# Kernel tuning notes

Hardware: AMD Instinct MI355X
Metric: run time of the kernel (lower is better)

Reference implementation:

```python
import jax, jax.numpy as jnp
import numpy as np

N = 50000        # nodes
E = 1_600_000    # edges
F_IN = 128
HID = 128
OUT = 128
NEG_SLOPE = 0.2  # PyG GATConv default


def _gat_layer(x, src, dst, W, a_src, a_dst, b, n_nodes):
    """PyG GATConv (heads=1, add_self_loops handled by caller)."""
    h = x @ W                                   # [N, d_out]
    alpha_src = h @ a_src                       # [N]
    alpha_dst = h @ a_dst                       # [N]
    e = jax.nn.leaky_relu(alpha_src[src] + alpha_dst[dst], NEG_SLOPE)  # [E']
    # segment softmax over incoming edges of each destination node
    m = jax.ops.segment_max(e, dst, num_segments=n_nodes)
    e = jnp.exp(e - m[dst])
    s = jax.ops.segment_sum(e, dst, num_segments=n_nodes)
    alpha = e / s[dst]                          # [E']
    out = jax.ops.segment_sum(alpha[:, None] * h[src], dst, num_segments=n_nodes)
    return out + b


def setup_inputs() -> dict:
    key = jax.random.key(0)
    ks = jax.random.split(key, 11)
    sW1 = 1.0 / np.sqrt(F_IN)
    sW2 = 1.0 / np.sqrt(HID)
    return {
        "x": jax.random.normal(ks[0], (N, F_IN), dtype=jnp.float32),
        "edge_index": jax.random.randint(ks[1], (2, E), 0, N, dtype=jnp.int64
                                         if jax.config.jax_enable_x64 else jnp.int32),
        "W1": jax.random.normal(ks[2], (F_IN, HID), dtype=jnp.float32) * sW1,
        "a1_src": jax.random.normal(ks[3], (HID,), dtype=jnp.float32) * sW2,
        "a1_dst": jax.random.normal(ks[4], (HID,), dtype=jnp.float32) * sW2,
        "b1": jnp.zeros((HID,), dtype=jnp.float32),
        "W2": jax.random.normal(ks[5], (HID, OUT), dtype=jnp.float32) * sW2,
        "a2_src": jax.random.normal(ks[6], (OUT,), dtype=jnp.float32) * sW2,
        "a2_dst": jax.random.normal(ks[7], (OUT,), dtype=jnp.float32) * sW2,
        "b2": jnp.zeros((OUT,), dtype=jnp.float32),
    }


def reference(x, edge_index, W1, a1_src, a1_dst, b1, W2, a2_src, a2_dst, b2):
    n = x.shape[0]
    loop = jnp.arange(n, dtype=edge_index.dtype)
    src = jnp.concatenate([edge_index[0], loop])   # add self loops (PyG default)
    dst = jnp.concatenate([edge_index[1], loop])
    h = _gat_layer(x, src, dst, W1, a1_src, a1_dst, b1, n)
    h = jax.nn.relu(h)
    # F.dropout with training=False is identity (eval-mode reference)
    out = _gat_layer(h, src, dst, W2, a2_src, a2_dst, b2, n)
    return out
```

## Files before the change

### kernel.cpp

```cpp
#include <hip/hip_runtime.h>
#include <hip/hip_bf16.h>
#include <hip/hip_fp16.h>

#define FD 128
#define CBW 128
#define NBK 512

typedef _Float16 half8 __attribute__((ext_vector_type(8)));
typedef float f32x4 __attribute__((ext_vector_type(4)));

__global__ __launch_bounds__(256) void k_wz(const float* __restrict__ W1,
                                            const float* __restrict__ W2,
                                            __half* __restrict__ T1,
                                            __half* __restrict__ T2,
                                            int* __restrict__ ccnt, int nb) {
    const int t = threadIdx.x;
    if (blockIdx.x == 2) {
        for (int i = t; i < nb; i += 256) ccnt[i] = 0;
        return;
    }
    __shared__ float sw[128 * 129];
    const float* W = blockIdx.x ? W2 : W1;
    __half* T = blockIdx.x ? T2 : T1;
#pragma unroll
    for (int i = 0; i < 64; i++) {
        int idx = i * 256 + t;
        sw[(idx >> 7) * 129 + (idx & 127)] = W[idx];
    }
    __syncthreads();
#pragma unroll
    for (int i = 0; i < 32; i++) {
        int o = i * 256 + t;
        int c = o >> 6, kp = o & 63;
        float lo = sw[(kp * 2) * 129 + c];
        float hi = sw[(kp * 2 + 1) * 129 + c];
        *(__half2*)&T[c * 128 + kp * 2] = __floats2half2_rn(lo, hi);
    }
}

__global__ __launch_bounds__(256) void k_pg(const int* __restrict__ dst,
                                            int* __restrict__ ccnt, int e, int nb,
                                            const float* __restrict__ X,
                                            const __half* __restrict__ Wt,
                                            const float* __restrict__ a_s,
                                            const float* __restrict__ a_d,
                                            __half* __restrict__ H,
                                            float* __restrict__ as_,
                                            float* __restrict__ ad_, int n) {
    __shared__ int lh[NBK];
    const int t = threadIdx.x;
    if (blockIdx.x < 256) {
        for (int i = t; i < NBK; i += 256) lh[i] = 0;
        __syncthreads();
        for (int i = blockIdx.x * 256 + t; i < e; i += 256 * 256)
            atomicAdd(&lh[dst[i] >> 7], 1);
        __syncthreads();
        for (int i = t; i < nb; i += 256) {
            int c = lh[i];
            if (c) atomicAdd(&ccnt[i], c);
        }
    } else {
        const int bid = blockIdx.x - 256;
        const int wave = t >> 6, lane = t & 63;
        const int g = lane >> 4, c16 = lane & 15;
        const int row0 = bid * 64 + wave * 16;

        half8 A[4];
        {
            int row = row0 + c16;
            int rc = (row < n) ? row : (n - 1);
            const float* xp = &X[(size_t)rc * 128 + g * 8];
#pragma unroll
            for (int kc = 0; kc < 4; kc++) {
                float4 x0 = *(const float4*)(xp + kc * 32);
                float4 x1 = *(const float4*)(xp + kc * 32 + 4);
                half8 a;
                a[0] = (_Float16)x0.x; a[1] = (_Float16)x0.y;
                a[2] = (_Float16)x0.z; a[3] = (_Float16)x0.w;
                a[4] = (_Float16)x1.x; a[5] = (_Float16)x1.y;
                a[6] = (_Float16)x1.z; a[7] = (_Float16)x1.w;
                A[kc] = a;
            }
        }
        f32x4 acc[8];
#pragma unroll
        for (int ct = 0; ct < 8; ct++) acc[ct] = (f32x4){0.f, 0.f, 0.f, 0.f};
#pragma unroll
        for (int ct = 0; ct < 8; ct++) {
            const __half* wp = &Wt[(ct * 16 + c16) * 128 + g * 8];
#pragma unroll
            for (int kc = 0; kc < 4; kc++) {
                half8 b = *(const half8*)(wp + kc * 32);
                acc[ct] = __builtin_amdgcn_mfma_f32_16x16x32_f16(A[kc], b, acc[ct], 0, 0, 0);
            }
        }
        float asv[8], adv[8];
#pragma unroll
        for (int ct = 0; ct < 8; ct++) {
            asv[ct] = a_s[ct * 16 + c16];
            adv[ct] = a_d[ct * 16 + c16];
        }
#pragma unroll
        for (int r = 0; r < 4; r++) {
            const int row = row0 + g * 4 + r;
            float vs = 0.f, vd = 0.f;
#pragma unroll
            for (int ct = 0; ct < 8; ct++) {
                float v = acc[ct][r];
                vs += v * asv[ct];
                vd += v * adv[ct];
                if (row < n) H[(size_t)row * 128 + ct * 16 + c16] = __float2half(v);
            }
#pragma unroll
            for (int off = 8; off; off >>= 1) {
                vs += __shfl_xor(vs, off, 16);
                vd += __shfl_xor(vd, off, 16);
            }
            if (c16 == 0 && row < n) { as_[row] = vs; ad_[row] = vd; }
        }
    }
}

__global__ void k_cscan(const int* __restrict__ ccnt, int* __restrict__ cbase,
                        int* __restrict__ ccur, int nb, int* __restrict__ rowptr, int n) {
    __shared__ int wsum[16];
    __shared__ int woff[17];
    const int t = threadIdx.x, lane = t & 63, wid = t >> 6;
    int v = (t < nb) ? ccnt[t] : 0;
    int s = v;
#pragma unroll
    for (int off = 1; off < 64; off <<= 1) {
        int u = __shfl_up(s, off, 64);
        if (lane >= off) s += u;
    }
    if (lane == 63) wsum[wid] = s;
    __syncthreads();
    if (wid == 0) {
        int w2 = (lane < 16) ? wsum[lane] : 0;
#pragma unroll
        for (int off = 1; off < 16; off <<= 1) {
            int u = __shfl_up(w2, off, 64);
            if (lane >= off) w2 += u;
        }
        if (lane < 16) woff[lane + 1] = w2;
        if (lane == 0) woff[0] = 0;
    }
    __syncthreads();
    int excl = woff[wid] + (s - v);
    if (t < nb) { cbase[t] = excl; ccur[t] = excl; }
    if (t == 0) { cbase[nb] = woff[16]; rowptr[n] = woff[16]; }
}

__global__ __launch_bounds__(256) void k_scat(const int* __restrict__ src,
                                              const int* __restrict__ dst,
                                              int* __restrict__ ccur,
                                              int* __restrict__ ebuf,
                                              int e, int nb, int nscat) {
    __shared__ int lh[NBK];
    __shared__ int lb[NBK];
    const int t = threadIdx.x;
    const int per = (e + nscat - 1) / nscat;
    const int lo = blockIdx.x * per;
    const int hi = min(e, lo + per);
    for (int i = t; i < NBK; i += 256) lh[i] = 0;
    __syncthreads();
    for (int i = lo + t; i < hi; i += 256) atomicAdd(&lh[dst[i] >> 7], 1);
    __syncthreads();
    for (int i = t; i < nb; i += 256) {
        int c = lh[i];
        lb[i] = c ? atomicAdd(&ccur[i], c) : 0;
    }
    __syncthreads();
    for (int i = t; i < NBK; i += 256) lh[i] = 0;
    __syncthreads();
    for (int i = lo + t; i < hi; i += 256) {
        int d = dst[i];
        int bkt = d >> 7;
        int r = atomicAdd(&lh[bkt], 1);
        ebuf[lb[bkt] + r] = (src[i] << 7) | (d & (CBW - 1));
    }
}

__global__ __launch_bounds__(256) void k_fine(const int* __restrict__ ebuf,
                                              const int* __restrict__ cbase,
                                              int* __restrict__ rowptr,
                                              int* __restrict__ colidx, int n) {
    const int b = blockIdx.x;
    const int node0 = b * CBW;
    const int nloc = min(CBW, n - node0);
    const int beg = cbase[b], end = cbase[b + 1];
    __shared__ int fh[CBW];
    __shared__ int fo[CBW];
    __shared__ int w0tot;
    const int t = threadIdx.x;
    if (t < CBW) fh[t] = 0;
    __syncthreads();
    for (int e = beg + t; e < end; e += 256) atomicAdd(&fh[ebuf[e] & (CBW - 1)], 1);
    __syncthreads();
    int v = 0, s = 0;
    if (t < CBW) {
        v = fh[t];
        s = v;
#pragma unroll
        for (int off = 1; off < 64; off <<= 1) {
            int u = __shfl_up(s, off, 64);
            if ((t & 63) >= off) s += u;
        }
        if (t == 63) w0tot = s;
    }
    __syncthreads();
    if (t < CBW) fo[t] = ((t >= 64) ? w0tot : 0) + s - v;
    __syncthreads();
    if (t < nloc) rowptr[node0 + t] = beg + fo[t];
    if (t < CBW) fh[t] = 0;
    __syncthreads();
    for (int e = beg + t; e < end; e += 256) {
        int rec = ebuf[e];
        int d = rec & (CBW - 1);
        int r = atomicAdd(&fh[d], 1);
        colidx[beg + fo[d] + r] = rec >> 7;
    }
}

__global__ __launch_bounds__(256) void k_gemm(const __half* __restrict__ X,
                                              const __half* __restrict__ Wt,
                                              const float* __restrict__ a_s,
                                              const float* __restrict__ a_d,
                                              __half* __restrict__ H,
                                              float* __restrict__ as_,
                                              float* __restrict__ ad_, int n) {
    const int t = threadIdx.x;
    const int wave = t >> 6, lane = t & 63;
    const int g = lane >> 4, c16 = lane & 15;
    const int row0 = blockIdx.x * 64 + wave * 16;

    half8 A[4];
    {
        int row = row0 + c16;
        int rc = (row < n) ? row : (n - 1);
        const __half* xp = &X[(size_t)rc * 128 + g * 8];
#pragma unroll
        for (int kc = 0; kc < 4; kc++) A[kc] = *(const half8*)(xp + kc * 32);
    }
    f32x4 acc[8];
#pragma unroll
    for (int ct = 0; ct < 8; ct++) acc[ct] = (f32x4){0.f, 0.f, 0.f, 0.f};
#pragma unroll
    for (int ct = 0; ct < 8; ct++) {
        const __half* wp = &Wt[(ct * 16 + c16) * 128 + g * 8];
#pragma unroll
        for (int kc = 0; kc < 4; kc++) {
            half8 b = *(const half8*)(wp + kc * 32);
            acc[ct] = __builtin_amdgcn_mfma_f32_16x16x32_f16(A[kc], b, acc[ct], 0, 0, 0);
        }
    }
    float asv[8], adv[8];
#pragma unroll
    for (int ct = 0; ct < 8; ct++) {
        asv[ct] = a_s[ct * 16 + c16];
        adv[ct] = a_d[ct * 16 + c16];
    }
#pragma unroll
    for (int r = 0; r < 4; r++) {
        const int row = row0 + g * 4 + r;
        float vs = 0.f, vd = 0.f;
#pragma unroll
        for (int ct = 0; ct < 8; ct++) {
            float v = acc[ct][r];
            vs += v * asv[ct];
            vd += v * adv[ct];
            if (row < n) H[(size_t)row * 128 + ct * 16 + c16] = __float2half(v);
        }
#pragma unroll
        for (int off = 8; off; off >>= 1) {
            vs += __shfl_xor(vs, off, 16);
            vd += __shfl_xor(vd, off, 16);
        }
        if (c16 == 0 && row < n) { as_[row] = vs; ad_[row] = vd; }
    }
}

__device__ __forceinline__ void fmix8(float* acc, uint4 hv, float w) {
    union { uint4 u; _Float16 h[8]; } c;
    c.u = hv;
#pragma unroll
    for (int j = 0; j < 8; j++) acc[j] += w * (float)c.h[j];
}

__global__ __launch_bounds__(256) void k_aggr(const __half* __restrict__ H,
                                              const float* __restrict__ as_,
                                              const float* __restrict__ ad_,
                                              const int* __restrict__ rowptr,
                                              const int* __restrict__ colidx,
                                              const float* __restrict__ bias,
                                              float* __restrict__ outf,
                                              __half* __restrict__ outh,
                                              int n, int mode) {
    __shared__ int2 pr[4][64];
    const int wid = threadIdx.x >> 6;
    const int lane = threadIdx.x & 63;
    const int node = blockIdx.x * 4 + wid;
    if (node >= n) return;
    const int q = lane >> 4;
    const int boff = (lane & 15) * 16;
    const char* Hb = (const char*)H + boff;
    const float adn = ad_[node];
    float sp = 0.f;
    float acc[8] = {0.f, 0.f, 0.f, 0.f, 0.f, 0.f, 0.f, 0.f};
    const int beg = rowptr[node], end = rowptr[node + 1];

    {
        float e = as_[node] + adn;
        e = (e > 0.f) ? e : 0.2f * e;
        const float w = __expf(e);
        if (lane == 63) sp += w;
        if (q == 3) {
            const uint4 hv = *(const uint4*)(Hb + ((unsigned)node << 8));
            fmix8(acc, hv, w);
        }
    }

    for (int it = beg; it < end; it += 64) {
        const int idx = it + lane;
        const bool valid = idx < end;
        const int sl = colidx[valid ? idx : (end - 1)];
        float e = as_[sl] + adn;
        e = (e > 0.f) ? e : 0.2f * e;
        const float w = valid ? __expf(e) : 0.f;
        sp += w;
        pr[wid][lane] = make_int2((int)((unsigned)sl << 8), __float_as_int(w));
        int m = end - it; if (m > 64) m = 64;
        const int iters = (m + 3) >> 2;
        int slot = q;
#pragma unroll 4
        for (int g = 0; g < iters; ++g) {
            const int2 p = pr[wid][slot];
            const float wg = __int_as_float(p.y);
            const uint4 hv = *(const uint4*)(Hb + (unsigned)p.x);
            fmix8(acc, hv, wg);
            slot += 4;
        }
    }

#pragma unroll
    for (int off = 1; off < 64; off <<= 1) sp += __shfl_xor(sp, off);
#pragma unroll
    for (int off = 16; off <= 32; off <<= 1) {
#pragma unroll
        for (int j = 0; j < 8; j++) acc[j] += __shfl_xor(acc[j], off);
    }
    if (q == 0) {
        const int f0 = boff >> 1;
        const float inv = 1.f / sp;
        float o[8];
        const float4 b0 = *(const float4*)&bias[f0];
        const float4 b1 = *(const float4*)&bias[f0 + 4];
        o[0] = acc[0] * inv + b0.x; o[1] = acc[1] * inv + b0.y;
        o[2] = acc[2] * inv + b0.z; o[3] = acc[3] * inv + b0.w;
        o[4] = acc[4] * inv + b1.x; o[5] = acc[5] * inv + b1.y;
        o[6] = acc[6] * inv + b1.z; o[7] = acc[7] * inv + b1.w;
        if (mode == 1) {
#pragma unroll
            for (int j = 0; j < 8; j++) o[j] = fmaxf(o[j], 0.f);
            union { __half2 h2[4]; uint4 u; } pkk;
            pkk.h2[0] = __floats2half2_rn(o[0], o[1]);
            pkk.h2[1] = __floats2half2_rn(o[2], o[3]);
            pkk.h2[2] = __floats2half2_rn(o[4], o[5]);
            pkk.h2[3] = __floats2half2_rn(o[6], o[7]);
            *(uint4*)&outh[(size_t)node * 128 + f0] = pkk.u;
        } else {
            *(float4*)&outf[(size_t)node * 128 + f0] = make_float4(o[0], o[1], o[2], o[3]);
            *(float4*)&outf[(size_t)node * 128 + f0 + 4] = make_float4(o[4], o[5], o[6], o[7]);
        }
    }
}

extern "C" void kernel_launch(void* const* d_in, const int* in_sizes, int n_in,
                              void* d_out, int out_size, void* d_ws, size_t ws_size,
                              hipStream_t stream) {
    const float* x   = (const float*)d_in[0];
    const int*   ei  = (const int*)d_in[1];
    const float* W1  = (const float*)d_in[2];
    const float* a1s = (const float*)d_in[3];
    const float* a1d = (const float*)d_in[4];
    const float* b1  = (const float*)d_in[5];
    const float* W2  = (const float*)d_in[6];
    const float* a2s = (const float*)d_in[7];
    const float* a2d = (const float*)d_in[8];
    const float* b2  = (const float*)d_in[9];
    float* dout = (float*)d_out;

    const int n = in_sizes[0] / FD;
    const int E = in_sizes[1] / 2;
    const int* src = ei;
    const int* dst = ei + E;
    const int NB = (n + CBW - 1) / CBW;

    char* base = (char*)d_ws;
    __half* buf0  = (__half*)base;
    int*    ebuf  = (int*)base;
    __half* H     = (__half*)(base + (size_t)n * FD * sizeof(__half));
    float* as_    = (float*)((char*)H + (size_t)n * FD * sizeof(__half));
    float* ad_    = as_ + n;
    int*   rowptr = (int*)(ad_ + n);
    int*   ccnt   = rowptr + (n + 1);
    int*   cbase  = ccnt + NB;
    int*   ccur   = cbase + NB + 1;
    int*   colidx = ccur + NB;
    size_t wt_off = (((size_t)((char*)(colidx + E) - base)) + 15) & ~(size_t)15;
    __half* Wt1h  = (__half*)(base + wt_off);
    __half* Wt2h  = Wt1h + 128 * 128;

    const int gemm_grid = (n + 63) / 64;
    const int node_grid = (n + 3) / 4;
    const int SCAT = 256;

    k_wz<<<3, 256, 0, stream>>>(W1, W2, Wt1h, Wt2h, ccnt, NB);
    k_pg<<<256 + gemm_grid, 256, 0, stream>>>(dst, ccnt, E, NB,
                                              x, Wt1h, a1s, a1d, H, as_, ad_, n);
    k_cscan<<<1, 1024, 0, stream>>>(ccnt, cbase, ccur, NB, rowptr, n);
    k_scat<<<SCAT, 256, 0, stream>>>(src, dst, ccur, ebuf, E, NB, SCAT);
    k_fine<<<NB, 256, 0, stream>>>(ebuf, cbase, rowptr, colidx, n);
    k_aggr<<<node_grid, 256, 0, stream>>>(H, as_, ad_, rowptr, colidx, b1,
                                          nullptr, buf0, n, 1);
    k_gemm<<<gemm_grid, 256, 0, stream>>>(buf0, Wt2h, a2s, a2d, H, as_, ad_, n);
    k_aggr<<<node_grid, 256, 0, stream>>>(H, as_, ad_, rowptr, colidx, b2,
                                          dout, nullptr, n, 0);
}
```

Baseline: 208.4 us.

## Split H into two feature halves and aggregate each half in separate blocks

H is now stored as two column-split planes of 64 features, [2][n][64] in fp16, and the aggregation grid is doubled so each block handles one half of the features for its nodes. Each gathered neighbor row becomes 128 bytes read by 8 lanes, with 8 edges processed in parallel per wave instead of 4. The goal is to shrink each gather's working set so it fits better in cache and to raise the number of edges in flight. In exchange, the per-edge softmax weights and the colidx reads are computed twice, once per half.

```diff
diff --git a/kernel.cpp b/kernel.cpp
--- a/kernel.cpp
+++ b/kernel.cpp
@@ -35,6 +35,56 @@
         float lo = sw[(kp * 2) * 129 + c];
         float hi = sw[(kp * 2 + 1) * 129 + c];
         *(__half2*)&T[c * 128 + kp * 2] = __floats2half2_rn(lo, hi);
+    }
+}
+
+__device__ __forceinline__ void gemm_core(const half8 A[4],
+                                          const __half* __restrict__ Wt,
+                                          const float* __restrict__ a_s,
+                                          const float* __restrict__ a_d,
+                                          __half* __restrict__ H,
+                                          float* __restrict__ as_,
+                                          float* __restrict__ ad_,
+                                          int n, int row0, int g, int c16) {
+    f32x4 acc[8];
+#pragma unroll
+    for (int ct = 0; ct < 8; ct++) acc[ct] = (f32x4){0.f, 0.f, 0.f, 0.f};
+#pragma unroll
+    for (int ct = 0; ct < 8; ct++) {
+        const __half* wp = &Wt[(ct * 16 + c16) * 128 + g * 8];
+#pragma unroll
+        for (int kc = 0; kc < 4; kc++) {
+            half8 b = *(const half8*)(wp + kc * 32);
+            acc[ct] = __builtin_amdgcn_mfma_f32_16x16x32_f16(A[kc], b, acc[ct], 0, 0, 0);
+        }
+    }
+    float asv[8], adv[8];
+#pragma unroll
+    for (int ct = 0; ct < 8; ct++) {
+        asv[ct] = a_s[ct * 16 + c16];
+        adv[ct] = a_d[ct * 16 + c16];
+    }
+#pragma unroll
+    for (int r = 0; r < 4; r++) {
+        const int row = row0 + g * 4 + r;
+        float vs = 0.f, vd = 0.f;
+#pragma unroll
+        for (int ct = 0; ct < 8; ct++) {
+            float v = acc[ct][r];
+            vs += v * asv[ct];
+            vd += v * adv[ct];
+            if (row < n) {
+                size_t hoff = (size_t)(ct >> 2) * ((size_t)n * 64)
+                            + (size_t)row * 64 + (ct & 3) * 16 + c16;
+                H[hoff] = __float2half(v);
+            }
+        }
+#pragma unroll
+        for (int off = 8; off; off >>= 1) {
+            vs += __shfl_xor(vs, off, 16);
+            vd += __shfl_xor(vd, off, 16);
+        }
+        if (c16 == 0 && row < n) { as_[row] = vs; ad_[row] = vd; }
     }
 }
 
@@ -64,7 +114,6 @@
         const int wave = t >> 6, lane = t & 63;
         const int g = lane >> 4, c16 = lane & 15;
         const int row0 = bid * 64 + wave * 16;
-
         half8 A[4];
         {
             int row = row0 + c16;
@@ -82,42 +131,7 @@
                 A[kc] = a;
             }
         }
-        f32x4 acc[8];
-#pragma unroll
-        for (int ct = 0; ct < 8; ct++) acc[ct] = (f32x4){0.f, 0.f, 0.f, 0.f};
-#pragma unroll
-        for (int ct = 0; ct < 8; ct++) {
-            const __half* wp = &Wt[(ct * 16 + c16) * 128 + g * 8];
-#pragma unroll
-            for (int kc = 0; kc < 4; kc++) {
-                half8 b = *(const half8*)(wp + kc * 32);
-                acc[ct] = __builtin_amdgcn_mfma_f32_16x16x32_f16(A[kc], b, acc[ct], 0, 0, 0);
-            }
-        }
-        float asv[8], adv[8];
-#pragma unroll
-        for (int ct = 0; ct < 8; ct++) {
-            asv[ct] = a_s[ct * 16 + c16];
-            adv[ct] = a_d[ct * 16 + c16];
-        }
-#pragma unroll
-        for (int r = 0; r < 4; r++) {
-            const int row = row0 + g * 4 + r;
-            float vs = 0.f, vd = 0.f;
-#pragma unroll
-            for (int ct = 0; ct < 8; ct++) {
-                float v = acc[ct][r];
-                vs += v * asv[ct];
-                vd += v * adv[ct];
-                if (row < n) H[(size_t)row * 128 + ct * 16 + c16] = __float2half(v);
-            }
-#pragma unroll
-            for (int off = 8; off; off >>= 1) {
-                vs += __shfl_xor(vs, off, 16);
-                vd += __shfl_xor(vd, off, 16);
-            }
-            if (c16 == 0 && row < n) { as_[row] = vs; ad_[row] = vd; }
-        }
+        gemm_core(A, Wt, a_s, a_d, H, as_, ad_, n, row0, g, c16);
     }
 }
 
@@ -233,7 +247,6 @@
     const int wave = t >> 6, lane = t & 63;
     const int g = lane >> 4, c16 = lane & 15;
     const int row0 = blockIdx.x * 64 + wave * 16;
-
     half8 A[4];
     {
         int row = row0 + c16;
@@ -242,42 +255,7 @@
 #pragma unroll
         for (int kc = 0; kc < 4; kc++) A[kc] = *(const half8*)(xp + kc * 32);
     }
-    f32x4 acc[8];
-#pragma unroll
-    for (int ct = 0; ct < 8; ct++) acc[ct] = (f32x4){0.f, 0.f, 0.f, 0.f};
-#pragma unroll
-    for (int ct = 0; ct < 8; ct++) {
-        const __half* wp = &Wt[(ct * 16 + c16) * 128 + g * 8];
-#pragma unroll
-        for (int kc = 0; kc < 4; kc++) {
-            half8 b = *(const half8*)(wp + kc * 32);
-            acc[ct] = __builtin_amdgcn_mfma_f32_16x16x32_f16(A[kc], b, acc[ct], 0, 0, 0);
-        }
-    }
-    float asv[8], adv[8];
-#pragma unroll
-    for (int ct = 0; ct < 8; ct++) {
-        asv[ct] = a_s[ct * 16 + c16];
-        adv[ct] = a_d[ct * 16 + c16];
-    }
-#pragma unroll
-    for (int r = 0; r < 4; r++) {
-        const int row = row0 + g * 4 + r;
-        float vs = 0.f, vd = 0.f;
-#pragma unroll
-        for (int ct = 0; ct < 8; ct++) {
-            float v = acc[ct][r];
-            vs += v * asv[ct];
-            vd += v * adv[ct];
-            if (row < n) H[(size_t)row * 128 + ct * 16 + c16] = __float2half(v);
-        }
-#pragma unroll
-        for (int off = 8; off; off >>= 1) {
-            vs += __shfl_xor(vs, off, 16);
-            vd += __shfl_xor(vd, off, 16);
-        }
-        if (c16 == 0 && row < n) { as_[row] = vs; ad_[row] = vd; }
-    }
+    gemm_core(A, Wt, a_s, a_d, H, as_, ad_, n, row0, g, c16);
 }
 
 __device__ __forceinline__ void fmix8(float* acc, uint4 hv, float w) {
@@ -297,13 +275,16 @@
                                               __half* __restrict__ outh,
                                               int n, int mode) {
     __shared__ int2 pr[4][64];
+    const int half = blockIdx.x & 1;
+    const int nblk = blockIdx.x >> 1;
     const int wid = threadIdx.x >> 6;
     const int lane = threadIdx.x & 63;
-    const int node = blockIdx.x * 4 + wid;
+    const int node = nblk * 4 + wid;
     if (node >= n) return;
-    const int q = lane >> 4;
-    const int boff = (lane & 15) * 16;
-    const char* Hb = (const char*)H + boff;
+    const int g8 = lane >> 3;
+    const int l8 = lane & 7;
+    const int boff = l8 * 16;
+    const char* Hb = (const char*)H + (size_t)half * ((size_t)n * 128) + boff;
     const float adn = ad_[node];
     float sp = 0.f;
     float acc[8] = {0.f, 0.f, 0.f, 0.f, 0.f, 0.f, 0.f, 0.f};
@@ -314,8 +295,8 @@
         e = (e > 0.f) ? e : 0.2f * e;
         const float w = __expf(e);
         if (lane == 63) sp += w;
-        if (q == 3) {
-            const uint4 hv = *(const uint4*)(Hb + ((unsigned)node << 8));
+        if (g8 == 7) {
+            const uint4 hv = *(const uint4*)(Hb + (unsigned)node * 128u);
             fmix8(acc, hv, w);
         }
     }
@@ -328,29 +309,29 @@
         e = (e > 0.f) ? e : 0.2f * e;
         const float w = valid ? __expf(e) : 0.f;
         sp += w;
-        pr[wid][lane] = make_int2((int)((unsigned)sl << 8), __float_as_int(w));
+        pr[wid][lane] = make_int2((int)((unsigned)sl * 128u), __float_as_int(w));
         int m = end - it; if (m > 64) m = 64;
-        const int iters = (m + 3) >> 2;
-        int slot = q;
+        const int iters = (m + 7) >> 3;
+        int slot = g8;
 #pragma unroll 4
         for (int g = 0; g < iters; ++g) {
             const int2 p = pr[wid][slot];
             const float wg = __int_as_float(p.y);
             const uint4 hv = *(const uint4*)(Hb + (unsigned)p.x);
             fmix8(acc, hv, wg);
-            slot += 4;
+            slot += 8;
         }
     }
 
 #pragma unroll
     for (int off = 1; off < 64; off <<= 1) sp += __shfl_xor(sp, off);
 #pragma unroll
-    for (int off = 16; off <= 32; off <<= 1) {
+    for (int off = 8; off <= 32; off <<= 1) {
 #pragma unroll
         for (int j = 0; j < 8; j++) acc[j] += __shfl_xor(acc[j], off);
     }
-    if (q == 0) {
-        const int f0 = boff >> 1;
+    if (g8 == 0) {
+        const int f0 = half * 64 + l8 * 8;
         const float inv = 1.f / sp;
         float o[8];
         const float4 b0 = *(const float4*)&bias[f0];
@@ -421,9 +402,9 @@
     k_cscan<<<1, 1024, 0, stream>>>(ccnt, cbase, ccur, NB, rowptr, n);
     k_scat<<<SCAT, 256, 0, stream>>>(src, dst, ccur, ebuf, E, NB, SCAT);
     k_fine<<<NB, 256, 0, stream>>>(ebuf, cbase, rowptr, colidx, n);
-    k_aggr<<<node_grid, 256, 0, stream>>>(H, as_, ad_, rowptr, colidx, b1,
-                                          nullptr, buf0, n, 1);
+    k_aggr<<<node_grid * 2, 256, 0, stream>>>(H, as_, ad_, rowptr, colidx, b1,
+                                              nullptr, buf0, n, 1);
     k_gemm<<<gemm_grid, 256, 0, stream>>>(buf0, Wt2h, a2s, a2d, H, as_, ad_, n);
-    k_aggr<<<node_grid, 256, 0, stream>>>(H, as_, ad_, rowptr, colidx, b2,
-                                          dout, nullptr, n, 0);
-}
+    k_aggr<<<node_grid * 2, 256, 0, stream>>>(H, as_, ad_, rowptr, colidx, b2,
+                                              dout, nullptr, n, 0);
+}
```

Result: slower. 223.8 us (+7.4%).
